# Kernel tuning notes

Hardware: AMD Instinct MI355X
Metric: run time of the kernel (lower is better)

The kernel has to match this reference:

```python
import jax, jax.numpy as jnp
import numpy as np

THRESHOLD = 0.5
ALPHA = 1.0
RATIO = 1.0
BACKGROUND = 0
OBJECT = 1


def cxcywh_to_xyxy(b):
    cxcy, wh = b[..., :2], b[..., 2:]
    return jnp.concatenate([cxcy - wh / 2.0, cxcy + wh / 2.0], axis=-1)


def xyxy_to_cxcywh(b):
    xy1, xy2 = b[..., :2], b[..., 2:]
    return jnp.concatenate([(xy1 + xy2) / 2.0, xy2 - xy1], axis=-1)


def cxcywh_to_gcxgcy(c, d):
    # standard SSD encoding with variances (0.1, 0.2)
    g_cxcy = (c[..., :2] - d[..., :2]) / (d[..., 2:] / 10.0)
    g_wh = jnp.log(c[..., 2:] / d[..., 2:]) * 5.0
    return jnp.concatenate([g_cxcy, g_wh], axis=-1)


def box_iou(a, b):
    # a: [M,4] xyxy, b: [A,4] xyxy -> [M,A]
    area_a = (a[:, 2] - a[:, 0]) * (a[:, 3] - a[:, 1])
    area_b = (b[:, 2] - b[:, 0]) * (b[:, 3] - b[:, 1])
    lt = jnp.maximum(a[:, None, :2], b[None, :, :2])
    rb = jnp.minimum(a[:, None, 2:], b[None, :, 2:])
    wh = jnp.clip(rb - lt, 0.0)
    inter = wh[..., 0] * wh[..., 1]
    return inter / (area_a[:, None] + area_b[None, :] - inter)


def setup_inputs() -> dict:
    B, A, M = 32, 16384, 64
    key = jax.random.key(0)
    k1, k2, k3, k4 = jax.random.split(key, 4)
    x = jax.random.normal(k1, (B, A, 4), dtype=jnp.float32)
    y = jax.random.normal(k2, (B, A, 2), dtype=jnp.float32)
    # valid xyxy GT boxes in [0,1]
    u = jax.random.uniform(k3, (B, M, 4), dtype=jnp.float32)
    xy1 = u[..., :2] * 0.7
    wh = 0.05 + u[..., 2:] * 0.25
    boxes = jnp.concatenate([xy1, xy1 + wh], axis=-1)
    # default (prior) boxes in cxcywh
    ud = jax.random.uniform(k4, (A, 4), dtype=jnp.float32)
    dcxcy = 0.05 + ud[..., :2] * 0.9
    dwh = 0.05 + ud[..., 2:] * 0.25
    default = jnp.concatenate([dcxcy, dwh], axis=-1)
    labels = jnp.ones((B, M), dtype=jnp.int32)  # all GT boxes are 'object'
    return {"x": x, "y": y, "boxes": boxes, "labels": labels, "default": default}


def reference(x, y, boxes, labels, default):
    B, A = x.shape[0], default.shape[0]
    M = boxes.shape[1]
    default_xy = cxcywh_to_xyxy(default)  # [A,4]

    def match(bx):  # bx: [M,4]
        iou = box_iou(bx, default_xy)              # [M,A]
        overlap = iou.max(axis=0)                  # [A] best GT per anchor
        digit = jnp.argmax(iou, axis=0)            # [A]
        best_anchor = jnp.argmax(iou, axis=1)      # [M] best anchor per GT
        digit = digit.at[best_anchor].set(jnp.arange(M))
        overlap = overlap.at[best_anchor].set(1.0)
        return digit, overlap

    digit, overlap = jax.vmap(match)(boxes)        # [B,A], [B,A]
    matched = jnp.take_along_axis(boxes, digit[..., None], axis=1)  # [B,A,4]
    localization = cxcywh_to_gcxgcy(xyxy_to_cxcywh(matched), default)  # [B,A,4]

    gathered = jnp.take_along_axis(labels, digit, axis=1)           # [B,A]
    classification = jnp.where(overlap < THRESHOLD, BACKGROUND, gathered)

    positives = classification == OBJECT
    total = positives.sum()
    totf = total.astype(x.dtype)

    # SmoothL1 (beta=1), mean over positive elements (P*4)
    d = x - localization
    ad = jnp.abs(d)
    sl1 = jnp.where(ad < 1.0, 0.5 * d * d, ad - 0.5)
    smooth = (sl1 * positives[..., None]).sum() / (totf * 4.0)

    # per-anchor cross entropy
    logp = jax.nn.log_softmax(y, axis=-1)                 # [B,A,2]
    ent = -jnp.take_along_axis(logp, classification[..., None], axis=-1)[..., 0]

    pos_sum = jnp.where(positives, ent, 0.0).sum()
    # hard negative mining: sort negatives descending, keep int(total*ratio)
    negv = jnp.where(positives, 0.0, ent).ravel()         # CE >= 0, so masking with 0 is safe
    neg_sorted = jnp.sort(negv)[::-1]
    keep = (totf * RATIO).astype(jnp.int32)
    neg_sum = jnp.where(jnp.arange(negv.shape[0]) < keep, neg_sorted, 0.0).sum()

    entropy = ALPHA * (pos_sum + neg_sum) / totf
    return smooth + entropy
```

## Files before the change

### kernel.cpp

```cpp
#include <hip/hip_runtime.h>

#define THRESH 0.5f

__global__ void k_zero(unsigned* __restrict__ p, int n) {
    int i = blockIdx.x * blockDim.x + threadIdx.x;
    if (i < n) p[i] = 0u;
}

__global__ void __launch_bounds__(256) k_matchboth(
        const float* __restrict__ boxes, const float* __restrict__ dflt,
        unsigned* __restrict__ match, unsigned long long* __restrict__ bestbox,
        int B, int A, int M, int chunks) {
    __shared__ float4 bx[128];
    __shared__ float barea[128];
    __shared__ float4 anch[256];
    __shared__ float adarea[256];
    __shared__ unsigned long long lm[128];
    int tid = threadIdx.x;
    int b = blockIdx.x / chunks;
    int chunk = blockIdx.x - b * chunks;
    int a = chunk * 256 + tid;
    if (tid < M) {
        float4 bv = *reinterpret_cast<const float4*>(boxes + ((size_t)b * M + tid) * 4);
        bx[tid] = bv;
        barea[tid] = (bv.z - bv.x) * (bv.w - bv.y);
        lm[tid] = 0ull;
    }
    bool aval = (a < A);
    float dx1 = 0.f, dy1 = 0.f, dx2 = 0.f, dy2 = 0.f, darea = 0.f;
    if (aval) {
        float4 dv = *reinterpret_cast<const float4*>(dflt + (size_t)a * 4);
        dx1 = dv.x - dv.z * 0.5f; dy1 = dv.y - dv.w * 0.5f;
        dx2 = dv.x + dv.z * 0.5f; dy2 = dv.y + dv.w * 0.5f;
        darea = (dx2 - dx1) * (dy2 - dy1);
    }
    anch[tid] = make_float4(dx1, dy1, dx2, dy2);
    adarea[tid] = darea;
    __syncthreads();
    if (aval) {
        float binter = -1.0f, bS = 1.0f; int bm = 0;
        #pragma unroll 4
        for (int m = 0; m < M; ++m) {
            float4 bb = bx[m];
            float lx = fmaxf(bb.x, dx1), ly = fmaxf(bb.y, dy1);
            float rx = fminf(bb.z, dx2), ry = fminf(bb.w, dy2);
            float w = fmaxf(rx - lx, 0.f), h = fmaxf(ry - ly, 0.f);
            float inter = w * h;
            float S = barea[m] + darea;
            bool gt = inter * bS > binter * S;
            binter = gt ? inter : binter;
            bS     = gt ? S : bS;
            bm     = gt ? m : bm;
        }
        unsigned fl = (3.0f * binter >= bS) ? (1u << 30) : 0u;
        match[(size_t)b * A + a] = (unsigned)bm | fl;
    }
    int wv = tid >> 6, lane = tid & 63;
    int abase = chunk * 256 + wv * 64;
    int kmax = min(64, A - abase);
    if (lane < M && kmax > 0) {
        float4 bb = bx[lane];
        float ba = barea[lane];
        float binter = -1.0f, bS = 1.0f; int bk = 0;
        #pragma unroll 4
        for (int k = 0; k < kmax; ++k) {
            float4 av = anch[wv * 64 + k];
            float lx = fmaxf(bb.x, av.x), ly = fmaxf(bb.y, av.y);
            float rx = fminf(bb.z, av.z), ry = fminf(bb.w, av.w);
            float w = fmaxf(rx - lx, 0.f), h = fmaxf(ry - ly, 0.f);
            float inter = w * h;
            float S = ba + adarea[wv * 64 + k];
            bool gt = inter * bS > binter * S;
            binter = gt ? inter : binter;
            bS     = gt ? S : bS;
            bk     = gt ? k : bk;
        }
        float best = binter / (bS - binter);
        atomicMax(&lm[lane], ((unsigned long long)__float_as_uint(best) << 32) |
                             (unsigned long long)(unsigned)(~(abase + bk)));
    }
    __syncthreads();
    if (tid < M) {
        unsigned long long p = lm[tid];
        if (p) atomicMax(&bestbox[(size_t)b * M + tid], p);
    }
}

__global__ void k_override(const unsigned long long* __restrict__ bestbox,
                           unsigned* __restrict__ match, int B, int A, int M) {
    int i = blockIdx.x * blockDim.x + threadIdx.x;
    if (i >= B * M) return;
    unsigned long long p = bestbox[i];
    unsigned a = ~(unsigned)(p & 0xFFFFFFFFull);
    if (a < (unsigned)A) {
        int b = i / M, m = i % M;
        atomicMax(&match[(size_t)b * A + a], 0x80000000u | (unsigned)m);
    }
}

__global__ void __launch_bounds__(256) k_main(
        const float* __restrict__ x, const float* __restrict__ y,
        const float* __restrict__ boxes, const int* __restrict__ labels,
        const float* __restrict__ dflt, const unsigned* __restrict__ match,
        float* __restrict__ negv, unsigned* __restrict__ hist1,
        unsigned* __restrict__ scal, int A, int M, int N) {
    __shared__ unsigned lh[2048];
    __shared__ float4 sbx[128];
    __shared__ int slab[128];
    int tid = threadIdx.x;
    int i0 = (blockIdx.x * 256 + tid) * 4;
    int b = (int)(((long long)blockIdx.x * 1024) / A);
    int a0 = i0 - b * A;
    uint4 w4 = *reinterpret_cast<const uint4*>(match + i0);
    const float4* yp = reinterpret_cast<const float4*>(y + (size_t)i0 * 2);
    float4 ya = yp[0], yb = yp[1];
    const float4* xp = reinterpret_cast<const float4*>(x + (size_t)i0 * 4);
    float4 xs[4] = {xp[0], xp[1], xp[2], xp[3]};
    const float4* dp = reinterpret_cast<const float4*>(dflt + (size_t)a0 * 4);
    float4 ds[4] = {dp[0], dp[1], dp[2], dp[3]};
    for (int j = tid; j < 2048; j += 256) lh[j] = 0u;
    if (tid < M) {
        sbx[tid] = *reinterpret_cast<const float4*>(boxes + ((size_t)b * M + tid) * 4);
        slab[tid] = labels[b * M + tid];
    }
    __syncthreads();
    float l_smooth = 0.f, l_pos = 0.f; int l_cnt = 0;
    {
        unsigned wws[4] = {w4.x, w4.y, w4.z, w4.w};
        float y0s[4] = {ya.x, ya.z, yb.x, yb.z};
        float y1s[4] = {ya.y, ya.w, yb.y, yb.w};
        float vs[4];
        #pragma unroll
        for (int e = 0; e < 4; ++e) {
            unsigned w = wws[e];
            int digit = (int)(w & 0xFFFFu);
            bool flag = (w & 0xC0000000u) != 0u;
            int c = flag ? slab[digit] : 0;
            bool pos = (c == 1);
            float4 bv = sbx[digit];
            float4 dv = ds[e];
            float cw = bv.z - bv.x, ch = bv.w - bv.y;
            float ccx = (bv.x + bv.z) * 0.5f, ccy = (bv.y + bv.w) * 0.5f;
            float l0 = (ccx - dv.x) / (dv.z * 0.1f);
            float l1 = (ccy - dv.y) / (dv.w * 0.1f);
            float l2 = logf(cw / dv.z) * 5.f;
            float l3 = logf(ch / dv.w) * 5.f;
            float4 xv = xs[e];
            float s = 0.f, d, ad;
            d = xv.x - l0; ad = fabsf(d); s += (ad < 1.f) ? 0.5f * d * d : ad - 0.5f;
            d = xv.y - l1; ad = fabsf(d); s += (ad < 1.f) ? 0.5f * d * d : ad - 0.5f;
            d = xv.z - l2; ad = fabsf(d); s += (ad < 1.f) ? 0.5f * d * d : ad - 0.5f;
            d = xv.w - l3; ad = fabsf(d); s += (ad < 1.f) ? 0.5f * d * d : ad - 0.5f;
            float y0 = y0s[e], y1v = y1s[e];
            float mx = fmaxf(y0, y1v);
            float lse = mx + log1pf(expf(-fabsf(y0 - y1v)));
            float ent = lse - ((c == 0) ? y0 : y1v);
            float v = pos ? 0.f : ent;
            vs[e] = v;
            if (pos) { l_smooth += s; l_pos += ent; l_cnt += 1; }
            atomicAdd(&lh[__float_as_uint(v) >> 21], 1u);
        }
        *reinterpret_cast<float4*>(negv + i0) = make_float4(vs[0], vs[1], vs[2], vs[3]);
    }
    for (int off = 32; off > 0; off >>= 1) {
        l_smooth += __shfl_down(l_smooth, off, 64);
        l_pos    += __shfl_down(l_pos, off, 64);
        l_cnt    += __shfl_down(l_cnt, off, 64);
    }
    __shared__ float rs[4], rp[4]; __shared__ int rc[4];
    int wv = tid >> 6;
    if ((tid & 63) == 0) { rs[wv] = l_smooth; rp[wv] = l_pos; rc[wv] = l_cnt; }
    __syncthreads();
    if (tid == 0) {
        float ss = rs[0] + rs[1] + rs[2] + rs[3];
        float pp = rp[0] + rp[1] + rp[2] + rp[3];
        int   cc = rc[0] + rc[1] + rc[2] + rc[3];
        if (ss != 0.f) atomicAdd((float*)&scal[2], ss);
        if (pp != 0.f) atomicAdd((float*)&scal[1], pp);
        if (cc)        atomicAdd((int*)&scal[0], cc);
    }
    __syncthreads();
    for (int j = tid; j < 2048; j += 256) {
        unsigned h = lh[j];
        if (h) atomicAdd(&hist1[j], h);
    }
}

__device__ __forceinline__ void scan_find(const unsigned* hist, int nbins,
                                          unsigned k, unsigned* ts, unsigned* res) {
    int t = threadIdx.x;
    int per = nbins >> 8;
    unsigned s = 0;
    for (int j = 0; j < per; ++j) s += hist[t * per + j];
    ts[t] = s;
    __syncthreads();
    for (int off = 1; off < 256; off <<= 1) {
        unsigned add = (t >= off) ? ts[t - off] : 0u;
        __syncthreads();
        ts[t] += add;
        __syncthreads();
    }
    unsigned total = ts[255];
    unsigned P = (t == 0) ? 0u : ts[t - 1];
    for (int j = 0; j < per; ++j) {
        unsigned h = hist[t * per + j];
        P += h;
        unsigned above = total - P;
        if (above < k && k <= above + h) { res[0] = (unsigned)(t * per + j); res[1] = k - above; }
    }
    __syncthreads();
}

__global__ void __launch_bounds__(256) k_refine2(
        const float* __restrict__ negv, int N, unsigned* __restrict__ scal,
        const unsigned* __restrict__ hist1, unsigned* __restrict__ hist2,
        float* __restrict__ fsum2, float* __restrict__ out) {
    __shared__ unsigned ts[256], res[2];
    __shared__ unsigned lh[2048];
    __shared__ float lf[2048];
    int tid = threadIdx.x;
    scan_find(hist1, 2048, scal[0], ts, res);
    unsigned bin1 = res[0], k1 = res[1];
    for (int j = tid; j < 2048; j += 256) { lh[j] = 0u; lf[j] = 0.f; }
    __syncthreads();
    float sacc = 0.f;
    int i = (blockIdx.x * 256 + tid) * 4;
    {
        float4 v4 = *reinterpret_cast<const float4*>(negv + i);
        float vv[4] = {v4.x, v4.y, v4.z, v4.w};
        #pragma unroll
        for (int e = 0; e < 4; ++e) {
            unsigned u = __float_as_uint(vv[e]);
            unsigned b1 = u >> 21;
            if (b1 > bin1) sacc += vv[e];
            else if (b1 == bin1) {
                unsigned j = (u >> 10) & 0x7FFu;
                atomicAdd(&lh[j], 1u);
                atomicAdd(&lf[j], vv[e]);
            }
        }
    }
    __syncthreads();
    for (int j = tid; j < 2048; j += 256) {
        unsigned h = lh[j];
        if (h) { atomicAdd(&hist2[j], h); atomicAdd(&fsum2[j], lf[j]); }
    }
    for (int off = 32; off > 0; off >>= 1) sacc += __shfl_down(sacc, off, 64);
    __shared__ float rsum[4];
    __shared__ unsigned isLast;
    int wv = tid >> 6;
    if ((tid & 63) == 0) rsum[wv] = sacc;
    __syncthreads();
    if (tid == 0) {
        float ss = rsum[0] + rsum[1] + rsum[2] + rsum[3];
        if (ss != 0.f) atomicAdd((float*)&scal[9], ss);
        __threadfence();
        unsigned prev = atomicAdd(&scal[12], 1u);
        isLast = (prev == gridDim.x - 1) ? 1u : 0u;
    }
    __syncthreads();
    if (!isLast) return;
    for (int j = tid; j < 2048; j += 256) {
        lh[j] = ((volatile unsigned*)hist2)[j];
        lf[j] = ((volatile float*)fsum2)[j];
    }
    __syncthreads();
    scan_find(lh, 2048, k1, ts, res);
    unsigned bin2 = res[0], k2 = res[1];
    float fs = 0.f;
    for (int j = tid; j < 2048; j += 256)
        if (j > (int)bin2) fs += lf[j];
    for (int off = 32; off > 0; off >>= 1) fs += __shfl_down(fs, off, 64);
    if ((tid & 63) == 0) rsum[wv] = fs;
    __syncthreads();
    if (tid == 0) {
        float fst = rsum[0] + rsum[1] + rsum[2] + rsum[3];
        volatile unsigned* vs = scal;
        volatile float* vf = (volatile float*)scal;
        float k = (float)vs[0];
        float tmid = __uint_as_float((bin1 << 21) | (bin2 << 10) | 512u);
        float neg_sum = vf[9] + fst + (float)k2 * tmid;
        float smooth = vf[2] / (k * 4.f);
        float ent = (vf[1] + neg_sum) / k;
        out[0] = smooth + ent;
    }
}

extern "C" void kernel_launch(void* const* d_in, const int* in_sizes, int n_in,
                              void* d_out, int out_size, void* d_ws, size_t ws_size,
                              hipStream_t stream) {
    const float* x      = (const float*)d_in[0];
    const float* y      = (const float*)d_in[1];
    const float* boxes  = (const float*)d_in[2];
    const int*   labels = (const int*)d_in[3];
    const float* dflt   = (const float*)d_in[4];
    float* out = (float*)d_out;

    int A = in_sizes[4] / 4;
    int B = in_sizes[1] / (2 * A);
    int M = in_sizes[3] / B;
    int N = B * A;
    int chunks = (A + 255) / 256;

    unsigned* ws    = (unsigned*)d_ws;
    unsigned* match = ws;
    float*    negv  = (float*)(ws + (size_t)N);
    unsigned long long* bestbox = (unsigned long long*)(ws + (size_t)2 * N);
    unsigned* hist1 = ws + (size_t)2 * N + 2 * B * M;
    unsigned* hist2 = hist1 + 2048;
    float*    fsum2 = (float*)(hist2 + 2048);
    unsigned* scal  = (unsigned*)(fsum2 + 2048);
    int nzero = 2 * B * M + 2048 * 3 + 16;

    k_zero<<<dim3((nzero + 255) / 256), dim3(256), 0, stream>>>(ws + (size_t)2 * N, nzero);
    k_matchboth<<<dim3(B * chunks), dim3(256), 0, stream>>>(boxes, dflt, match, bestbox, B, A, M, chunks);
    k_override<<<dim3((B * M + 255) / 256), dim3(256), 0, stream>>>(bestbox, match, B, A, M);
    k_main<<<dim3(N / 1024), dim3(256), 0, stream>>>(x, y, boxes, labels, dflt, match,
                                                     negv, hist1, scal, A, M, N);
    k_refine2<<<dim3(N / 1024), dim3(256), 0, stream>>>(negv, N, scal, hist1, hist2, fsum2, out);
}
```

Measured before the change: 146.9 us.

## Fuse best-anchor override into main kernel and process eight anchors per thread

Removes the separate override kernel. Each k_main block now reads the per-GT best anchors and applies the forced matches through a shared-memory override table covering its own 2048 anchors. It also doubles the work per thread in k_main and k_refine2 to eight elements, halving the grid sizes. This saves one kernel launch and the global atomics, and gives each thread more loads in flight. The cost is higher register pressure, extra shared memory and fewer blocks. The flag mask changes to 0x40000000 because the override bit is no longer written into match.

```diff
diff --git a/kernel.cpp b/kernel.cpp
--- a/kernel.cpp
+++ b/kernel.cpp
@@ -86,55 +86,65 @@
     }
 }
 
-__global__ void k_override(const unsigned long long* __restrict__ bestbox,
-                           unsigned* __restrict__ match, int B, int A, int M) {
-    int i = blockIdx.x * blockDim.x + threadIdx.x;
-    if (i >= B * M) return;
-    unsigned long long p = bestbox[i];
-    unsigned a = ~(unsigned)(p & 0xFFFFFFFFull);
-    if (a < (unsigned)A) {
-        int b = i / M, m = i % M;
-        atomicMax(&match[(size_t)b * A + a], 0x80000000u | (unsigned)m);
-    }
-}
-
 __global__ void __launch_bounds__(256) k_main(
         const float* __restrict__ x, const float* __restrict__ y,
         const float* __restrict__ boxes, const int* __restrict__ labels,
         const float* __restrict__ dflt, const unsigned* __restrict__ match,
+        const unsigned long long* __restrict__ bestbox,
         float* __restrict__ negv, unsigned* __restrict__ hist1,
         unsigned* __restrict__ scal, int A, int M, int N) {
     __shared__ unsigned lh[2048];
     __shared__ float4 sbx[128];
     __shared__ int slab[128];
+    __shared__ int ovr[2048];
     int tid = threadIdx.x;
-    int i0 = (blockIdx.x * 256 + tid) * 4;
-    int b = (int)(((long long)blockIdx.x * 1024) / A);
+    int i0 = (blockIdx.x * 256 + tid) * 8;
+    int base = blockIdx.x * 2048;
+    int b = (int)(((long long)blockIdx.x * 2048) / A);
     int a0 = i0 - b * A;
-    uint4 w4 = *reinterpret_cast<const uint4*>(match + i0);
+    const uint4* mp = reinterpret_cast<const uint4*>(match + i0);
+    uint4 w4a = mp[0], w4b = mp[1];
     const float4* yp = reinterpret_cast<const float4*>(y + (size_t)i0 * 2);
-    float4 ya = yp[0], yb = yp[1];
+    float4 yv[4];
+    #pragma unroll
+    for (int e = 0; e < 4; ++e) yv[e] = yp[e];
     const float4* xp = reinterpret_cast<const float4*>(x + (size_t)i0 * 4);
-    float4 xs[4] = {xp[0], xp[1], xp[2], xp[3]};
+    float4 xs[8];
+    #pragma unroll
+    for (int e = 0; e < 8; ++e) xs[e] = xp[e];
     const float4* dp = reinterpret_cast<const float4*>(dflt + (size_t)a0 * 4);
-    float4 ds[4] = {dp[0], dp[1], dp[2], dp[3]};
-    for (int j = tid; j < 2048; j += 256) lh[j] = 0u;
+    float4 ds[8];
+    #pragma unroll
+    for (int e = 0; e < 8; ++e) ds[e] = dp[e];
+    for (int j = tid; j < 2048; j += 256) { lh[j] = 0u; ovr[j] = -1; }
     if (tid < M) {
         sbx[tid] = *reinterpret_cast<const float4*>(boxes + ((size_t)b * M + tid) * 4);
         slab[tid] = labels[b * M + tid];
     }
     __syncthreads();
+    if (tid < M) {
+        unsigned long long p = bestbox[(size_t)b * M + tid];
+        unsigned a = ~(unsigned)(p & 0xFFFFFFFFull);
+        if (a < (unsigned)A) {
+            int target = b * A + (int)a;
+            if (target >= base && target < base + 2048)
+                atomicMax(&ovr[target - base], tid);
+        }
+    }
+    __syncthreads();
     float l_smooth = 0.f, l_pos = 0.f; int l_cnt = 0;
     {
-        unsigned wws[4] = {w4.x, w4.y, w4.z, w4.w};
-        float y0s[4] = {ya.x, ya.z, yb.x, yb.z};
-        float y1s[4] = {ya.y, ya.w, yb.y, yb.w};
-        float vs[4];
+        unsigned wws[8] = {w4a.x, w4a.y, w4a.z, w4a.w, w4b.x, w4b.y, w4b.z, w4b.w};
+        float y0s[8] = {yv[0].x, yv[0].z, yv[1].x, yv[1].z, yv[2].x, yv[2].z, yv[3].x, yv[3].z};
+        float y1s[8] = {yv[0].y, yv[0].w, yv[1].y, yv[1].w, yv[2].y, yv[2].w, yv[3].y, yv[3].w};
+        float vs[8];
         #pragma unroll
-        for (int e = 0; e < 4; ++e) {
+        for (int e = 0; e < 8; ++e) {
             unsigned w = wws[e];
             int digit = (int)(w & 0xFFFFu);
-            bool flag = (w & 0xC0000000u) != 0u;
+            bool flag = (w & 0x40000000u) != 0u;
+            int o = ovr[tid * 8 + e];
+            if (o >= 0) { digit = o; flag = true; }
             int c = flag ? slab[digit] : 0;
             bool pos = (c == 1);
             float4 bv = sbx[digit];
@@ -160,7 +170,9 @@
             if (pos) { l_smooth += s; l_pos += ent; l_cnt += 1; }
             atomicAdd(&lh[__float_as_uint(v) >> 21], 1u);
         }
-        *reinterpret_cast<float4*>(negv + i0) = make_float4(vs[0], vs[1], vs[2], vs[3]);
+        float4* np = reinterpret_cast<float4*>(negv + i0);
+        np[0] = make_float4(vs[0], vs[1], vs[2], vs[3]);
+        np[1] = make_float4(vs[4], vs[5], vs[6], vs[7]);
     }
     for (int off = 32; off > 0; off >>= 1) {
         l_smooth += __shfl_down(l_smooth, off, 64);
@@ -219,17 +231,18 @@
     __shared__ unsigned lh[2048];
     __shared__ float lf[2048];
     int tid = threadIdx.x;
+    int i = (blockIdx.x * 256 + tid) * 8;
+    const float4* vp = reinterpret_cast<const float4*>(negv + i);
+    float4 va = vp[0], vb = vp[1];
     scan_find(hist1, 2048, scal[0], ts, res);
     unsigned bin1 = res[0], k1 = res[1];
     for (int j = tid; j < 2048; j += 256) { lh[j] = 0u; lf[j] = 0.f; }
     __syncthreads();
     float sacc = 0.f;
-    int i = (blockIdx.x * 256 + tid) * 4;
     {
-        float4 v4 = *reinterpret_cast<const float4*>(negv + i);
-        float vv[4] = {v4.x, v4.y, v4.z, v4.w};
+        float vv[8] = {va.x, va.y, va.z, va.w, vb.x, vb.y, vb.z, vb.w};
         #pragma unroll
-        for (int e = 0; e < 4; ++e) {
+        for (int e = 0; e < 8; ++e) {
             unsigned u = __float_as_uint(vv[e]);
             unsigned b1 = u >> 21;
             if (b1 > bin1) sacc += vv[e];
@@ -275,9 +288,9 @@
     __syncthreads();
     if (tid == 0) {
         float fst = rsum[0] + rsum[1] + rsum[2] + rsum[3];
-        volatile unsigned* vs = scal;
+        volatile unsigned* vsc = scal;
         volatile float* vf = (volatile float*)scal;
-        float k = (float)vs[0];
+        float k = (float)vsc[0];
         float tmid = __uint_as_float((bin1 << 21) | (bin2 << 10) | 512u);
         float neg_sum = vf[9] + fst + (float)k2 * tmid;
         float smooth = vf[2] / (k * 4.f);
@@ -314,8 +327,7 @@
 
     k_zero<<<dim3((nzero + 255) / 256), dim3(256), 0, stream>>>(ws + (size_t)2 * N, nzero);
     k_matchboth<<<dim3(B * chunks), dim3(256), 0, stream>>>(boxes, dflt, match, bestbox, B, A, M, chunks);
-    k_override<<<dim3((B * M + 255) / 256), dim3(256), 0, stream>>>(bestbox, match, B, A, M);
-    k_main<<<dim3(N / 1024), dim3(256), 0, stream>>>(x, y, boxes, labels, dflt, match,
+    k_main<<<dim3(N / 2048), dim3(256), 0, stream>>>(x, y, boxes, labels, dflt, match, bestbox,
                                                      negv, hist1, scal, A, M, N);
-    k_refine2<<<dim3(N / 1024), dim3(256), 0, stream>>>(negv, N, scal, hist1, hist2, fsum2, out);
-}
+    k_refine2<<<dim3(N / 2048), dim3(256), 0, stream>>>(negv, N, scal, hist1, hist2, fsum2, out);
+}
```

Result: faster. 134.4 us (-8.5%).
